# Optimization experiments

Measured on AMD Instinct MI355X. Metric: run time of the kernel, lower is better.

Reference implementation:

```python
import jax, jax.numpy as jnp
import numpy as np
from jax import lax

HIDDEN = 2048
VOCAB = 7
MAX_LENGTH = 1024


def setup_inputs() -> dict:
    key = jax.random.key(0)
    ks = jax.random.split(key, 8)
    s = 0.02  # small init scale, mimics trained-weight magnitude
    return {
        "h0": jax.random.normal(ks[0], (1, HIDDEN), jnp.float32),
        "c0": jax.random.normal(ks[1], (1, HIDDEN), jnp.float32),
        "W_ih": jax.random.normal(ks[2], (4 * HIDDEN, VOCAB), jnp.float32) * s,
        "W_hh": jax.random.normal(ks[3], (4 * HIDDEN, HIDDEN), jnp.float32) * s,
        "b_ih": jax.random.normal(ks[4], (4 * HIDDEN,), jnp.float32) * s,
        "b_hh": jax.random.normal(ks[5], (4 * HIDDEN,), jnp.float32) * s,
        "W_out": jax.random.normal(ks[6], (VOCAB, HIDDEN), jnp.float32) * s,
        "b_out": jax.random.normal(ks[7], (VOCAB,), jnp.float32) * s,
    }


def reference(h0, c0, W_ih, W_hh, b_ih, b_hh, W_out, b_out):
    H = h0.shape[-1]
    V = W_out.shape[0]
    # initial decoder input: one-hot at index V-1 (SOS), shape [1, V]
    x0 = jnp.zeros((1, V), h0.dtype).at[0, V - 1].set(1.0)

    def step(carry, _):
        x, h, c = carry
        xr = jax.nn.relu(x)
        # PyTorch LSTM: gates = x W_ih^T + b_ih + h W_hh^T + b_hh, order i,f,g,o
        gates = xr @ W_ih.T + b_ih + h @ W_hh.T + b_hh  # [1, 4H]
        i, f, g, o = jnp.split(gates, 4, axis=-1)
        c2 = jax.nn.sigmoid(f) * c + jax.nn.sigmoid(i) * jnp.tanh(g)
        h2 = jax.nn.sigmoid(o) * jnp.tanh(c2)
        logits = h2 @ W_out.T + b_out  # [1, V]
        # greedy feedback: one-hot of argmax (topk(1) equivalent)
        nxt = jax.nn.one_hot(jnp.argmax(logits, axis=-1), V, dtype=h0.dtype)
        return (nxt, h2, c2), logits[0]

    (_, hN, cN), outs = lax.scan(step, (x0, h0, c0), None, length=MAX_LENGTH)
    log_probs = jax.nn.log_softmax(outs, axis=-1)  # [MAX_LENGTH, V]
    return log_probs, hN, cN
```

## Files before the change

### kernel.cpp

```cpp
#include <hip/hip_runtime.h>
#include <hip/hip_cooperative_groups.h>

namespace cg = cooperative_groups;

#define HIDDEN   2048
#define VOCAB    7
#define STEPS    1024
#define NBLOCKS  512
#define NTHREADS 256
#define NWAVES   (NTHREADS / 64)
#define FAN      8
#define NLEAF    (NBLOCKS / FAN)
#define NMID     (NLEAF / FAN)

typedef unsigned long long u64;

__device__ __align__(256) float g_h[3][HIDDEN];
__device__ __align__(256) float g_p0[NLEAF][64];
__device__ __align__(256) float g_p1[NMID][64];
__device__ __align__(256) float g_p2[64];
__device__ __align__(256) int   g_c0[NLEAF * 32];
__device__ __align__(256) int   g_c1[NMID * 32];
__device__ __align__(256) int   g_c2[32];
__device__ __align__(256) u64   g_pub[8 * 16];
__device__ float g_c[HIDDEN];
__device__ float g_partfb[NBLOCKS * VOCAB];
__device__ int   g_xi;

__device__ __forceinline__ float sigm(float x) { return 1.0f / (1.0f + expf(-x)); }

#define LOAD_AG(p)     __hip_atomic_load((p), __ATOMIC_RELAXED, __HIP_MEMORY_SCOPE_AGENT)
#define STORE_AG(p, v) __hip_atomic_store((p), (v), __ATOMIC_RELAXED, __HIP_MEMORY_SCOPE_AGENT)
#define RMW_ADD_AG(p)  __hip_atomic_fetch_add((p), 1, __ATOMIC_RELAXED, __HIP_MEMORY_SCOPE_AGENT)
#define VM_DRAIN()     asm volatile("s_waitcnt vmcnt(0)" ::: "memory")
#define C_FENCE()      asm volatile("" ::: "memory")

__device__ __forceinline__ float4 h_pair(const u64* h8, int m) {
    u64 lo = LOAD_AG((u64*)&h8[2 * m]);
    u64 hi = LOAD_AG((u64*)&h8[2 * m + 1]);
    float4 r;
    r.x = __uint_as_float((unsigned)lo);
    r.y = __uint_as_float((unsigned)(lo >> 32));
    r.z = __uint_as_float((unsigned)hi);
    r.w = __uint_as_float((unsigned)(hi >> 32));
    return r;
}

__device__ __forceinline__ float sel7(const float w[VOCAB], int xi) {
    float r = w[0];
    #pragma unroll
    for (int v = 1; v < VOCAB; ++v) r = (xi == v) ? w[v] : r;
    return r;
}

__device__ __forceinline__ float slot_reduce(float x) {
    x += __shfl_down(x, 28, 64);
    x += __shfl_down(x, 14, 64);
    x += __shfl_down(x, 7, 64);
    return x;
}

__global__ __launch_bounds__(NTHREADS, 2)
void coop_kernel(const float* __restrict__ h0,  const float* __restrict__ c0,
                 const float* __restrict__ W_ih, const float* __restrict__ W_hh,
                 const float* __restrict__ b_ih, const float* __restrict__ b_hh,
                 const float* __restrict__ W_out, const float* __restrict__ b_out,
                 float* __restrict__ out)
{
    cg::grid_group grid = cg::this_grid();
    const int tid  = threadIdx.x;
    const int gid  = blockIdx.x * NTHREADS + tid;
    const int lane = tid & 63;
    const int wib  = tid >> 6;
    const int j    = blockIdx.x * NWAVES + wib;

    const int leaf  = blockIdx.x >> 3;
    const int slot0 = blockIdx.x & 7;
    const int mid   = leaf >> 3;
    const int slot1 = leaf & 7;
    const int slot2 = mid;
    const int rep   = blockIdx.x >> 6;

    __shared__ float s_part[NWAVES][VOCAB];
    __shared__ u64   s_gx;

    if (gid < HIDDEN) STORE_AG(&g_h[0][gid], h0[gid]);
    if (blockIdx.x == 0) {
        if (tid < NLEAF) STORE_AG(&g_c0[tid * 32], 0);
        if (tid < NMID)  STORE_AG(&g_c1[tid * 32], 0);
        if (tid == 0)    STORE_AG(&g_c2[0], 0);
        if (tid < 8)     STORE_AG(&g_pub[tid * 16], (u64)0);
    }

    const float4* Wr0 = (const float4*)(W_hh + (size_t)j * HIDDEN);
    const float4* Wr1 = (const float4*)(W_hh + (size_t)(j + HIDDEN) * HIDDEN);
    const float4* Wr2 = (const float4*)(W_hh + (size_t)(j + 2 * HIDDEN) * HIDDEN);
    const float4* Wr3 = (const float4*)(W_hh + (size_t)(j + 3 * HIDDEN) * HIDDEN);

    float bsum0 = 0.f, bsum1 = 0.f, bsum2 = 0.f, bsum3 = 0.f;
    float cv = 0.f, h_fin = 0.f;
    float wih0[VOCAB], wih1[VOCAB], wih2[VOCAB], wih3[VOCAB];
    if (lane == 0) {
        bsum0 = b_ih[j]              + b_hh[j];
        bsum1 = b_ih[j + HIDDEN]     + b_hh[j + HIDDEN];
        bsum2 = b_ih[j + 2 * HIDDEN] + b_hh[j + 2 * HIDDEN];
        bsum3 = b_ih[j + 3 * HIDDEN] + b_hh[j + 3 * HIDDEN];
        cv = c0[j];
        #pragma unroll
        for (int v = 0; v < VOCAB; ++v) {
            wih0[v] = W_ih[(size_t)j * VOCAB + v];
            wih1[v] = W_ih[(size_t)(j + HIDDEN) * VOCAB + v];
            wih2[v] = W_ih[(size_t)(j + 2 * HIDDEN) * VOCAB + v];
            wih3[v] = W_ih[(size_t)(j + 3 * HIDDEN) * VOCAB + v];
        }
    }
    const float wout = (lane < VOCAB) ? W_out[lane * HIDDEN + j] : 0.0f;
    float bov[VOCAB];
    #pragma unroll
    for (int v = 0; v < VOCAB; ++v) bov[v] = b_out[v];

    grid.sync();

    int xi = VOCAB - 1;
    int rb = 0, wbuf = 1;

    for (int t = 0; t < STEPS; ++t) {
        const u64* h8 = (const u64*)g_h[rb];

        float4 hreg[8];
        #pragma unroll
        for (int it = 0; it < 8; ++it) hreg[it] = h_pair(h8, it * 64 + lane);

        float a0 = 0.f, a1 = 0.f, a2 = 0.f, a3 = 0.f;
        #pragma unroll
        for (int it = 0; it < 8; ++it) {
            const float4 hv = hreg[it];
            const float4 w0 = Wr0[it * 64 + lane];
            const float4 w1 = Wr1[it * 64 + lane];
            const float4 w2 = Wr2[it * 64 + lane];
            const float4 w3 = Wr3[it * 64 + lane];
            a0 += w0.x * hv.x + w0.y * hv.y + w0.z * hv.z + w0.w * hv.w;
            a1 += w1.x * hv.x + w1.y * hv.y + w1.z * hv.z + w1.w * hv.w;
            a2 += w2.x * hv.x + w2.y * hv.y + w2.z * hv.z + w2.w * hv.w;
            a3 += w3.x * hv.x + w3.y * hv.y + w3.z * hv.z + w3.w * hv.w;
        }
        #pragma unroll
        for (int off = 32; off > 0; off >>= 1) {
            a0 += __shfl_down(a0, off, 64);
            a1 += __shfl_down(a1, off, 64);
            a2 += __shfl_down(a2, off, 64);
            a3 += __shfl_down(a3, off, 64);
        }

        float h2v = 0.0f;
        if (lane == 0) {
            const float gi = a0 + bsum0 + sel7(wih0, xi);
            const float gf = a1 + bsum1 + sel7(wih1, xi);
            const float gg = a2 + bsum2 + sel7(wih2, xi);
            const float go = a3 + bsum3 + sel7(wih3, xi);
            cv  = sigm(gf) * cv + sigm(gi) * tanhf(gg);
            h2v = sigm(go) * tanhf(cv);
            h_fin = h2v;
            STORE_AG(&g_h[wbuf][j], h2v);
        }
        h2v = __shfl(h2v, 0, 64);

        if (lane < VOCAB) s_part[wib][lane] = h2v * wout;
        __syncthreads();

        if (wib == 0) {
            if (lane < VOCAB)
                STORE_AG(&g_p0[leaf][slot0 * VOCAB + lane],
                         s_part[0][lane] + s_part[1][lane] + s_part[2][lane] + s_part[3][lane]);
            VM_DRAIN();
            int old0 = 0;
            if (lane == 0) old0 = RMW_ADD_AG(&g_c0[leaf * 32]);
            old0 = __shfl(old0, 0, 64);
            C_FENCE();
            if (old0 == (t + 1) * FAN - 1) {
                float x = (lane < FAN * VOCAB) ? LOAD_AG(&g_p0[leaf][lane]) : 0.0f;
                x = slot_reduce(x);
                if (lane < VOCAB) STORE_AG(&g_p1[mid][slot1 * VOCAB + lane], x);
                VM_DRAIN();
                int old1 = 0;
                if (lane == 0) old1 = RMW_ADD_AG(&g_c1[mid * 32]);
                old1 = __shfl(old1, 0, 64);
                C_FENCE();
                if (old1 == (t + 1) * FAN - 1) {
                    float y = (lane < FAN * VOCAB) ? LOAD_AG(&g_p1[mid][lane]) : 0.0f;
                    y = slot_reduce(y);
                    if (lane < VOCAB) STORE_AG(&g_p2[slot2 * VOCAB + lane], y);
                    VM_DRAIN();
                    int old2 = 0;
                    if (lane == 0) old2 = RMW_ADD_AG(&g_c2[0]);
                    old2 = __shfl(old2, 0, 64);
                    C_FENCE();
                    if (old2 == (t + 1) * FAN - 1) {
                        float z = (lane < FAN * VOCAB) ? LOAD_AG(&g_p2[lane]) : 0.0f;
                        z = slot_reduce(z);
                        float l[VOCAB];
                        #pragma unroll
                        for (int v = 0; v < VOCAB; ++v) l[v] = __shfl(z, v, 64);
                        if (lane == 0) {
                            float mx = -1e30f;
                            #pragma unroll
                            for (int v = 0; v < VOCAB; ++v) { l[v] += bov[v]; mx = fmaxf(mx, l[v]); }
                            float se = 0.0f;
                            #pragma unroll
                            for (int v = 0; v < VOCAB; ++v) se += expf(l[v] - mx);
                            const float lse = mx + logf(se);
                            int am = 0; float best = l[0];
                            #pragma unroll
                            for (int v = 1; v < VOCAB; ++v) if (l[v] > best) { best = l[v]; am = v; }
                            #pragma unroll
                            for (int v = 0; v < VOCAB; ++v) out[t * VOCAB + v] = l[v] - lse;
                            const u64 val = ((u64)(unsigned)(t + 1) << 32) | (u64)(unsigned)am;
                            #pragma unroll
                            for (int r = 0; r < 8; ++r) STORE_AG(&g_pub[r * 16], val);
                        }
                    }
                }
            }
        }

        if (t + 1 < STEPS) {
            if (tid == 0) {
                u64 cur = LOAD_AG(&g_pub[rep * 16]);
                while ((unsigned)(cur >> 32) != (unsigned)(t + 1)) {
                    __builtin_amdgcn_s_sleep(2);
                    cur = LOAD_AG(&g_pub[rep * 16]);
                }
                s_gx = cur;
            }
            C_FENCE();
            __syncthreads();
            xi = (int)(unsigned)s_gx;
        }
        rb = wbuf;
        wbuf = (wbuf + 1 == 3) ? 0 : wbuf + 1;
    }

    if (lane == 0) {
        out[STEPS * VOCAB + j]          = h_fin;
        out[STEPS * VOCAB + HIDDEN + j] = cv;
    }
}

__global__ __launch_bounds__(NTHREADS)
void fb_init(const float* __restrict__ h0, const float* __restrict__ c0) {
    int gid = blockIdx.x * NTHREADS + threadIdx.x;
    if (gid < HIDDEN) { g_h[0][gid] = h0[gid]; g_c[gid] = c0[gid]; }
    if (gid == 0) g_xi = VOCAB - 1;
}

__global__ __launch_bounds__(NTHREADS, 2)
void fb_step(const float* __restrict__ W_ih, const float* __restrict__ W_hh,
             const float* __restrict__ b_ih, const float* __restrict__ b_hh,
             const float* __restrict__ W_out, int t)
{
    const int tid  = threadIdx.x;
    const int lane = tid & 63;
    const int wib  = tid >> 6;
    const int j    = blockIdx.x * NWAVES + wib;

    __shared__ float s_part[NWAVES][VOCAB];

    const float4* h4 = (const float4*)g_h[t & 1];
    const float4* Wr0 = (const float4*)(W_hh + (size_t)j * HIDDEN);
    const float4* Wr1 = (const float4*)(W_hh + (size_t)(j + HIDDEN) * HIDDEN);
    const float4* Wr2 = (const float4*)(W_hh + (size_t)(j + 2 * HIDDEN) * HIDDEN);
    const float4* Wr3 = (const float4*)(W_hh + (size_t)(j + 3 * HIDDEN) * HIDDEN);

    float a0 = 0.f, a1 = 0.f, a2 = 0.f, a3 = 0.f;
    #pragma unroll
    for (int it = 0; it < 8; ++it) {
        const float4 hv = h4[it * 64 + lane];
        const float4 w0 = Wr0[it * 64 + lane];
        const float4 w1 = Wr1[it * 64 + lane];
        const float4 w2 = Wr2[it * 64 + lane];
        const float4 w3 = Wr3[it * 64 + lane];
        a0 += w0.x * hv.x + w0.y * hv.y + w0.z * hv.z + w0.w * hv.w;
        a1 += w1.x * hv.x + w1.y * hv.y + w1.z * hv.z + w1.w * hv.w;
        a2 += w2.x * hv.x + w2.y * hv.y + w2.z * hv.z + w2.w * hv.w;
        a3 += w3.x * hv.x + w3.y * hv.y + w3.z * hv.z + w3.w * hv.w;
    }
    #pragma unroll
    for (int off = 32; off > 0; off >>= 1) {
        a0 += __shfl_down(a0, off, 64);
        a1 += __shfl_down(a1, off, 64);
        a2 += __shfl_down(a2, off, 64);
        a3 += __shfl_down(a3, off, 64);
    }

    float h2v = 0.0f;
    if (lane == 0) {
        const int xi = g_xi;
        const float gi = a0 + b_ih[j] + b_hh[j] + W_ih[j * VOCAB + xi];
        const float gf = a1 + b_ih[j + HIDDEN] + b_hh[j + HIDDEN] + W_ih[(j + HIDDEN) * VOCAB + xi];
        const float gg = a2 + b_ih[j + 2 * HIDDEN] + b_hh[j + 2 * HIDDEN] + W_ih[(j + 2 * HIDDEN) * VOCAB + xi];
        const float go = a3 + b_ih[j + 3 * HIDDEN] + b_hh[j + 3 * HIDDEN] + W_ih[(j + 3 * HIDDEN) * VOCAB + xi];
        const float cv = sigm(gf) * g_c[j] + sigm(gi) * tanhf(gg);
        h2v = sigm(go) * tanhf(cv);
        g_c[j] = cv;
        g_h[(t + 1) & 1][j] = h2v;
    }
    h2v = __shfl(h2v, 0, 64);

    const float wout = (lane < VOCAB) ? W_out[lane * HIDDEN + j] : 0.0f;
    if (lane < VOCAB) s_part[wib][lane] = h2v * wout;
    __syncthreads();
    if (tid < VOCAB)
        g_partfb[blockIdx.x * VOCAB + tid] =
            s_part[0][tid] + s_part[1][tid] + s_part[2][tid] + s_part[3][tid];
}

__global__ void fb_logits(const float* __restrict__ b_out, float* __restrict__ out, int t) {
    const int lane = threadIdx.x;
    float lg[VOCAB];
    #pragma unroll
    for (int v = 0; v < VOCAB; ++v) {
        float s = 0.0f;
        for (int i = lane; i < NBLOCKS; i += 64) s += g_partfb[i * VOCAB + v];
        #pragma unroll
        for (int off = 32; off > 0; off >>= 1) s += __shfl_down(s, off, 64);
        lg[v] = s;
    }
    if (lane == 0) {
        float l[VOCAB];
        float mx = -1e30f;
        #pragma unroll
        for (int v = 0; v < VOCAB; ++v) { l[v] = lg[v] + b_out[v]; mx = fmaxf(mx, l[v]); }
        float se = 0.0f;
        #pragma unroll
        for (int v = 0; v < VOCAB; ++v) se += expf(l[v] - mx);
        const float lse = mx + logf(se);
        int am = 0; float best = l[0];
        #pragma unroll
        for (int v = 1; v < VOCAB; ++v) if (l[v] > best) { best = l[v]; am = v; }
        #pragma unroll
        for (int v = 0; v < VOCAB; ++v) out[t * VOCAB + v] = l[v] - lse;
        g_xi = am;
    }
}

__global__ __launch_bounds__(NTHREADS)
void fb_fin(float* __restrict__ out) {
    int gid = blockIdx.x * NTHREADS + threadIdx.x;
    if (gid < HIDDEN) {
        out[STEPS * VOCAB + gid]          = g_h[0][gid];
        out[STEPS * VOCAB + HIDDEN + gid] = g_c[gid];
    }
}

extern "C" void kernel_launch(void* const* d_in, const int* in_sizes, int n_in,
                              void* d_out, int out_size, void* d_ws, size_t ws_size,
                              hipStream_t stream)
{
    const float* h0    = (const float*)d_in[0];
    const float* c0    = (const float*)d_in[1];
    const float* W_ih  = (const float*)d_in[2];
    const float* W_hh  = (const float*)d_in[3];
    const float* b_ih  = (const float*)d_in[4];
    const float* b_hh  = (const float*)d_in[5];
    const float* W_out = (const float*)d_in[6];
    const float* b_out = (const float*)d_in[7];
    float* out = (float*)d_out;

    void* args[] = { &h0, &c0, &W_ih, &W_hh, &b_ih, &b_hh, &W_out, &b_out, &out };
    hipError_t e = hipLaunchCooperativeKernel((void*)coop_kernel,
                                              dim3(NBLOCKS), dim3(NTHREADS), args, 0, stream);
    if (e != hipSuccess) {
        fb_init<<<HIDDEN / NTHREADS, NTHREADS, 0, stream>>>(h0, c0);
        for (int t = 0; t < STEPS; ++t) {
            fb_step<<<NBLOCKS, NTHREADS, 0, stream>>>(W_ih, W_hh, b_ih, b_hh, W_out, t);
            fb_logits<<<1, 64, 0, stream>>>(b_out, out, t);
        }
        fb_fin<<<HIDDEN / NTHREADS, NTHREADS, 0, stream>>>(out);
    }
}
```

Measured before the change: 7.733 ms.

## Recompute output logits redundantly per block instead of tree-reducing partials

Each block's first wave now computes the full W_out·h logits for the previous step from the h vector it already loads, then derives argmax locally. The global partial-sum tree reduction and the broadcast of the argmax are gone. The barrier tree keeps only counters plus an integer step flag, and block 0 writes the log-softmax output one step late, with a final epilogue for the last step. This shortens the serial critical path per step, at the cost of 7×2048 redundant multiply-adds and extra W_out reads in every block.

```diff
diff --git a/kernel.cpp b/kernel.cpp
--- a/kernel.cpp
+++ b/kernel.cpp
@@ -16,13 +16,10 @@
 typedef unsigned long long u64;
 
 __device__ __align__(256) float g_h[3][HIDDEN];
-__device__ __align__(256) float g_p0[NLEAF][64];
-__device__ __align__(256) float g_p1[NMID][64];
-__device__ __align__(256) float g_p2[64];
 __device__ __align__(256) int   g_c0[NLEAF * 32];
 __device__ __align__(256) int   g_c1[NMID * 32];
 __device__ __align__(256) int   g_c2[32];
-__device__ __align__(256) u64   g_pub[8 * 16];
+__device__ __align__(256) int   g_pubi[8 * 32];
 __device__ float g_c[HIDDEN];
 __device__ float g_partfb[NBLOCKS * VOCAB];
 __device__ int   g_xi;
@@ -32,7 +29,6 @@
 #define LOAD_AG(p)     __hip_atomic_load((p), __ATOMIC_RELAXED, __HIP_MEMORY_SCOPE_AGENT)
 #define STORE_AG(p, v) __hip_atomic_store((p), (v), __ATOMIC_RELAXED, __HIP_MEMORY_SCOPE_AGENT)
 #define RMW_ADD_AG(p)  __hip_atomic_fetch_add((p), 1, __ATOMIC_RELAXED, __HIP_MEMORY_SCOPE_AGENT)
-#define VM_DRAIN()     asm volatile("s_waitcnt vmcnt(0)" ::: "memory")
 #define C_FENCE()      asm volatile("" ::: "memory")
 
 __device__ __forceinline__ float4 h_pair(const u64* h8, int m) {
@@ -51,13 +47,6 @@
     #pragma unroll
     for (int v = 1; v < VOCAB; ++v) r = (xi == v) ? w[v] : r;
     return r;
-}
-
-__device__ __forceinline__ float slot_reduce(float x) {
-    x += __shfl_down(x, 28, 64);
-    x += __shfl_down(x, 14, 64);
-    x += __shfl_down(x, 7, 64);
-    return x;
 }
 
 __global__ __launch_bounds__(NTHREADS, 2)
@@ -74,22 +63,18 @@
     const int wib  = tid >> 6;
     const int j    = blockIdx.x * NWAVES + wib;
 
-    const int leaf  = blockIdx.x >> 3;
-    const int slot0 = blockIdx.x & 7;
-    const int mid   = leaf >> 3;
-    const int slot1 = leaf & 7;
-    const int slot2 = mid;
-    const int rep   = blockIdx.x >> 6;
-
-    __shared__ float s_part[NWAVES][VOCAB];
-    __shared__ u64   s_gx;
+    const int leaf = blockIdx.x >> 3;
+    const int mid  = leaf >> 3;
+    const int rep  = blockIdx.x >> 6;
+
+    __shared__ int s_xi;
 
     if (gid < HIDDEN) STORE_AG(&g_h[0][gid], h0[gid]);
     if (blockIdx.x == 0) {
         if (tid < NLEAF) STORE_AG(&g_c0[tid * 32], 0);
         if (tid < NMID)  STORE_AG(&g_c1[tid * 32], 0);
         if (tid == 0)    STORE_AG(&g_c2[0], 0);
-        if (tid < 8)     STORE_AG(&g_pub[tid * 16], (u64)0);
+        if (tid < 8)     STORE_AG(&g_pubi[tid * 32], 0);
     }
 
     const float4* Wr0 = (const float4*)(W_hh + (size_t)j * HIDDEN);
@@ -114,14 +99,12 @@
             wih3[v] = W_ih[(size_t)(j + 3 * HIDDEN) * VOCAB + v];
         }
     }
-    const float wout = (lane < VOCAB) ? W_out[lane * HIDDEN + j] : 0.0f;
     float bov[VOCAB];
     #pragma unroll
     for (int v = 0; v < VOCAB; ++v) bov[v] = b_out[v];
 
     grid.sync();
 
-    int xi = VOCAB - 1;
     int rb = 0, wbuf = 1;
 
     for (int t = 0; t < STEPS; ++t) {
@@ -130,6 +113,45 @@
         float4 hreg[8];
         #pragma unroll
         for (int it = 0; it < 8; ++it) hreg[it] = h_pair(h8, it * 64 + lane);
+
+        if (wib == 0) {
+            if (t > 0) {
+                float lg[VOCAB];
+                #pragma unroll
+                for (int v = 0; v < VOCAB; ++v) {
+                    const float4* Wo = (const float4*)(W_out + (size_t)v * HIDDEN);
+                    float acc = 0.f;
+                    #pragma unroll
+                    for (int it = 0; it < 8; ++it) {
+                        const float4 w = Wo[it * 64 + lane];
+                        const float4 hv = hreg[it];
+                        acc += w.x * hv.x + w.y * hv.y + w.z * hv.z + w.w * hv.w;
+                    }
+                    #pragma unroll
+                    for (int off = 32; off > 0; off >>= 1) acc += __shfl_down(acc, off, 64);
+                    lg[v] = acc;
+                }
+                if (lane == 0) {
+                    float mx = -1e30f;
+                    #pragma unroll
+                    for (int v = 0; v < VOCAB; ++v) { lg[v] += bov[v]; mx = fmaxf(mx, lg[v]); }
+                    int am = 0; float best = lg[0];
+                    #pragma unroll
+                    for (int v = 1; v < VOCAB; ++v) if (lg[v] > best) { best = lg[v]; am = v; }
+                    s_xi = am;
+                    if (blockIdx.x == 0) {
+                        float se = 0.0f;
+                        #pragma unroll
+                        for (int v = 0; v < VOCAB; ++v) se += expf(lg[v] - mx);
+                        const float lse = mx + logf(se);
+                        #pragma unroll
+                        for (int v = 0; v < VOCAB; ++v) out[(t - 1) * VOCAB + v] = lg[v] - lse;
+                    }
+                }
+            } else if (lane == 0) {
+                s_xi = VOCAB - 1;
+            }
+        }
 
         float a0 = 0.f, a1 = 0.f, a2 = 0.f, a3 = 0.f;
         #pragma unroll
@@ -152,6 +174,9 @@
             a3 += __shfl_down(a3, off, 64);
         }
 
+        __syncthreads();
+        const int xi = s_xi;
+
         float h2v = 0.0f;
         if (lane == 0) {
             const float gi = a0 + bsum0 + sel7(wih0, xi);
@@ -163,83 +188,69 @@
             h_fin = h2v;
             STORE_AG(&g_h[wbuf][j], h2v);
         }
-        h2v = __shfl(h2v, 0, 64);
-
-        if (lane < VOCAB) s_part[wib][lane] = h2v * wout;
+
         __syncthreads();
 
-        if (wib == 0) {
-            if (lane < VOCAB)
-                STORE_AG(&g_p0[leaf][slot0 * VOCAB + lane],
-                         s_part[0][lane] + s_part[1][lane] + s_part[2][lane] + s_part[3][lane]);
-            VM_DRAIN();
-            int old0 = 0;
-            if (lane == 0) old0 = RMW_ADD_AG(&g_c0[leaf * 32]);
-            old0 = __shfl(old0, 0, 64);
-            C_FENCE();
+        if (wib == 0 && lane == 0) {
+            const int old0 = RMW_ADD_AG(&g_c0[leaf * 32]);
             if (old0 == (t + 1) * FAN - 1) {
-                float x = (lane < FAN * VOCAB) ? LOAD_AG(&g_p0[leaf][lane]) : 0.0f;
-                x = slot_reduce(x);
-                if (lane < VOCAB) STORE_AG(&g_p1[mid][slot1 * VOCAB + lane], x);
-                VM_DRAIN();
-                int old1 = 0;
-                if (lane == 0) old1 = RMW_ADD_AG(&g_c1[mid * 32]);
-                old1 = __shfl(old1, 0, 64);
-                C_FENCE();
+                const int old1 = RMW_ADD_AG(&g_c1[mid * 32]);
                 if (old1 == (t + 1) * FAN - 1) {
-                    float y = (lane < FAN * VOCAB) ? LOAD_AG(&g_p1[mid][lane]) : 0.0f;
-                    y = slot_reduce(y);
-                    if (lane < VOCAB) STORE_AG(&g_p2[slot2 * VOCAB + lane], y);
-                    VM_DRAIN();
-                    int old2 = 0;
-                    if (lane == 0) old2 = RMW_ADD_AG(&g_c2[0]);
-                    old2 = __shfl(old2, 0, 64);
-                    C_FENCE();
+                    const int old2 = RMW_ADD_AG(&g_c2[0]);
                     if (old2 == (t + 1) * FAN - 1) {
-                        float z = (lane < FAN * VOCAB) ? LOAD_AG(&g_p2[lane]) : 0.0f;
-                        z = slot_reduce(z);
-                        float l[VOCAB];
                         #pragma unroll
-                        for (int v = 0; v < VOCAB; ++v) l[v] = __shfl(z, v, 64);
-                        if (lane == 0) {
-                            float mx = -1e30f;
-                            #pragma unroll
-                            for (int v = 0; v < VOCAB; ++v) { l[v] += bov[v]; mx = fmaxf(mx, l[v]); }
-                            float se = 0.0f;
-                            #pragma unroll
-                            for (int v = 0; v < VOCAB; ++v) se += expf(l[v] - mx);
-                            const float lse = mx + logf(se);
-                            int am = 0; float best = l[0];
-                            #pragma unroll
-                            for (int v = 1; v < VOCAB; ++v) if (l[v] > best) { best = l[v]; am = v; }
-                            #pragma unroll
-                            for (int v = 0; v < VOCAB; ++v) out[t * VOCAB + v] = l[v] - lse;
-                            const u64 val = ((u64)(unsigned)(t + 1) << 32) | (u64)(unsigned)am;
-                            #pragma unroll
-                            for (int r = 0; r < 8; ++r) STORE_AG(&g_pub[r * 16], val);
-                        }
+                        for (int r = 0; r < 8; ++r) STORE_AG(&g_pubi[r * 32], t + 1);
                     }
                 }
             }
         }
 
-        if (t + 1 < STEPS) {
-            if (tid == 0) {
-                u64 cur = LOAD_AG(&g_pub[rep * 16]);
-                while ((unsigned)(cur >> 32) != (unsigned)(t + 1)) {
-                    __builtin_amdgcn_s_sleep(2);
-                    cur = LOAD_AG(&g_pub[rep * 16]);
-                }
-                s_gx = cur;
+        if (tid == 0) {
+            int cur = LOAD_AG(&g_pubi[rep * 32]);
+            while (cur < t + 1) {
+                __builtin_amdgcn_s_sleep(1);
+                cur = LOAD_AG(&g_pubi[rep * 32]);
             }
-            C_FENCE();
-            __syncthreads();
-            xi = (int)(unsigned)s_gx;
-        }
+        }
+        C_FENCE();
+        __syncthreads();
+
         rb = wbuf;
         wbuf = (wbuf + 1 == 3) ? 0 : wbuf + 1;
     }
 
+    if (blockIdx.x == 0 && wib == 0) {
+        const u64* h8 = (const u64*)g_h[rb];
+        float4 hreg[8];
+        #pragma unroll
+        for (int it = 0; it < 8; ++it) hreg[it] = h_pair(h8, it * 64 + lane);
+        float lg[VOCAB];
+        #pragma unroll
+        for (int v = 0; v < VOCAB; ++v) {
+            const float4* Wo = (const float4*)(W_out + (size_t)v * HIDDEN);
+            float acc = 0.f;
+            #pragma unroll
+            for (int it = 0; it < 8; ++it) {
+                const float4 w = Wo[it * 64 + lane];
+                const float4 hv = hreg[it];
+                acc += w.x * hv.x + w.y * hv.y + w.z * hv.z + w.w * hv.w;
+            }
+            #pragma unroll
+            for (int off = 32; off > 0; off >>= 1) acc += __shfl_down(acc, off, 64);
+            lg[v] = acc;
+        }
+        if (lane == 0) {
+            float mx = -1e30f;
+            #pragma unroll
+            for (int v = 0; v < VOCAB; ++v) { lg[v] += bov[v]; mx = fmaxf(mx, lg[v]); }
+            float se = 0.0f;
+            #pragma unroll
+            for (int v = 0; v < VOCAB; ++v) se += expf(lg[v] - mx);
+            const float lse = mx + logf(se);
+            #pragma unroll
+            for (int v = 0; v < VOCAB; ++v) out[(STEPS - 1) * VOCAB + v] = lg[v] - lse;
+        }
+    }
     if (lane == 0) {
         out[STEPS * VOCAB + j]          = h_fin;
         out[STEPS * VOCAB + HIDDEN + j] = cv;
```

New measurement: 13.83 ms. 78.9% more time.
